# Kernel optimization log

Hardware: AMD Instinct MI355X
Metric: run time of the kernel (lower is better)

Reference implementation:

```python
import jax, jax.numpy as jnp
import numpy as np

B, LQ, LK, D = 8, 2048, 2048, 128
NEG = -100000.0


def setup_inputs() -> dict:
    key = jax.random.key(0)
    kq, kk, kv, km = jax.random.split(key, 4)
    q = jax.random.normal(kq, (B, LQ, D), dtype=jnp.float32)
    k = jax.random.normal(kk, (B, LK, D), dtype=jnp.float32)
    v = jax.random.normal(kv, (B, LK, D), dtype=jnp.float32)
    mask = jax.random.randint(km, (B, LQ, LK), 0, 2, dtype=jnp.int32)
    return {"q": q, "k": k, "v": v, "mask": mask}


def reference(q, k, v, mask):
    # atten_score = q @ k^T / sqrt(d)   [B, Lq, Lk]
    scores = jnp.einsum("bqd,bkd->bqk", q, k) / jnp.sqrt(jnp.float32(q.shape[-1]))
    # mask_mod == 2: additive mask, masked positions pushed to large negative
    scores = scores + mask.astype(jnp.float32) * NEG
    # sigmoid instead of softmax (no normalization across keys)
    attn = jax.nn.sigmoid(scores)
    return jnp.einsum("bqk,bkd->bqd", attn, v)
```

## Files before the change

### kernel.cpp

```cpp
#include <hip/hip_runtime.h>
#include <hip/hip_bf16.h>

#define B_   8
#define LQ_  2048
#define LK_  2048
#define D_   128
#define QBLK 64
#define KBLK 64
#define THREADS 512
#define SCALE 0.08838834764831845f
#define NEGL2E (-1.44269504088896340736f * SCALE)

typedef __attribute__((ext_vector_type(8))) __bf16 bf16x8;
typedef __attribute__((ext_vector_type(4))) float  f32x4;
typedef __attribute__((ext_vector_type(4))) float  fx4;
typedef __attribute__((ext_vector_type(4))) int    i32x4;

__global__ __launch_bounds__(256)
void kprep(const float* __restrict__ k, __bf16* __restrict__ kb)
{
    size_t i = ((size_t)blockIdx.x * 256 + threadIdx.x) * 8;
    fx4 a = *(const fx4*)(k + i);
    fx4 b = *(const fx4*)(k + i + 4);
    bf16x8 w;
#pragma unroll
    for (int j = 0; j < 4; ++j) { w[j] = (__bf16)a[j]; w[4 + j] = (__bf16)b[j]; }
    *(bf16x8*)(kb + i) = w;
}

__global__ __launch_bounds__(128)
void vprep(const float* __restrict__ v, __bf16* __restrict__ vt)
{
    const int b  = blockIdx.x & 7;
    const int k0 = (blockIdx.x >> 3) * 64;
    const int d  = threadIdx.x;
    const float* vb = v + ((size_t)b * LK_ + k0) * D_ + d;
    __bf16* vr = vt + ((size_t)b * D_ + d) * LK_ + k0;
#pragma unroll
    for (int grp = 0; grp < 2; ++grp) {
#pragma unroll
        for (int g = 0; g < 4; ++g) {
            bf16x8 w;
#pragma unroll
            for (int e = 0; e < 8; ++e) {
                int h = e >> 2, j = e & 3;
                int key = grp * 32 + h * 16 + g * 4 + j;
                w[e] = (__bf16)vb[(size_t)key * D_];
            }
            *(bf16x8*)(vr + grp * 32 + g * 8) = w;
        }
    }
}

__global__ __launch_bounds__(THREADS, 2)
void sigattn_main(const float* __restrict__ q, const int* __restrict__ mask,
                  const __bf16* __restrict__ Kb, const __bf16* __restrict__ Vt,
                  float* __restrict__ out)
{
    __shared__ float red[64 * 132];

    const int tid  = threadIdx.x;
    const int lane = tid & 63;
    const int l15  = lane & 15;
    const int g    = lane >> 4;
    const int wid  = tid >> 6;
    const int qg   = wid & 1;
    const int kg   = (wid >> 1) & 1;
    const int tp   = wid >> 2;

    const int bid   = blockIdx.x;
    const int b     = bid & 7;
    const int q0    = (bid >> 3) * QBLK;
    const int qbase = qg * 32;

    const float*  qb = q    + ((size_t)b * LQ_ + q0) * D_;
    const int*    mb = mask + ((size_t)b * LQ_ + q0) * LK_;
    const __bf16* kb = Kb   + (size_t)b * LK_ * D_;
    const __bf16* vt = Vt   + (size_t)b * D_ * LK_;
    float*        ob = out  + ((size_t)b * LQ_ + q0) * D_;

    bf16x8 qfrag[2][4];
#pragma unroll
    for (int qq = 0; qq < 2; ++qq) {
        const float* qrow = qb + (size_t)(qbase + qq * 16 + l15) * D_;
#pragma unroll
        for (int dblk = 0; dblk < 4; ++dblk) {
            fx4 f0 = *(const fx4*)(qrow + dblk * 32 + g * 8);
            fx4 f1 = *(const fx4*)(qrow + dblk * 32 + g * 8 + 4);
            bf16x8 w;
#pragma unroll
            for (int j = 0; j < 4; ++j) { w[j] = (__bf16)f0[j]; w[4 + j] = (__bf16)f1[j]; }
            qfrag[qq][dblk] = w;
        }
    }

    f32x4 oacc[2][8];
#pragma unroll
    for (int qq = 0; qq < 2; ++qq)
#pragma unroll
        for (int nb = 0; nb < 8; ++nb) oacc[qq][nb] = (f32x4){0.f, 0.f, 0.f, 0.f};

    const int* mr[2];
    mr[0] = mb + (size_t)(qbase + l15) * LK_ + kg * 32 + 4 * g;
    mr[1] = mr[0] + (size_t)16 * LK_;

    int kt = tp * KBLK;
    i32x4 mcur[2][2];
#pragma unroll
    for (int qq = 0; qq < 2; ++qq)
#pragma unroll
        for (int ksl = 0; ksl < 2; ++ksl)
            mcur[qq][ksl] = __builtin_nontemporal_load((const i32x4*)(mr[qq] + kt + ksl * 16));

    for (int i = 0; i < 16; ++i, kt += 2 * KBLK) {
        const int ktp = (i < 15) ? kt + 2 * KBLK : kt;

        i32x4 mnxt[2][2];
#pragma unroll
        for (int qq = 0; qq < 2; ++qq)
#pragma unroll
            for (int ksl = 0; ksl < 2; ++ksl)
                mnxt[qq][ksl] = __builtin_nontemporal_load((const i32x4*)(mr[qq] + ktp + ksl * 16));

        bf16x8 kfr[2][4];
#pragma unroll
        for (int ksl = 0; ksl < 2; ++ksl)
#pragma unroll
            for (int dblk = 0; dblk < 4; ++dblk)
                kfr[ksl][dblk] = *(const bf16x8*)(kb + (size_t)(kt + kg * 32 + ksl * 16 + l15) * D_ + dblk * 32 + g * 8);

        bf16x8 vfr[8];
#pragma unroll
        for (int nb = 0; nb < 8; ++nb)
            vfr[nb] = *(const bf16x8*)(vt + (size_t)(nb * 16 + l15) * LK_ + kt + kg * 32 + g * 8);

        f32x4 sacc[2][2];
#pragma unroll
        for (int qq = 0; qq < 2; ++qq)
#pragma unroll
            for (int ksl = 0; ksl < 2; ++ksl)
                sacc[qq][ksl] = (f32x4){0.f, 0.f, 0.f, 0.f};
#pragma unroll
        for (int ksl = 0; ksl < 2; ++ksl)
#pragma unroll
            for (int dblk = 0; dblk < 4; ++dblk) {
                bf16x8 a = kfr[ksl][dblk];
#pragma unroll
                for (int qq = 0; qq < 2; ++qq)
                    sacc[qq][ksl] = __builtin_amdgcn_mfma_f32_16x16x32_bf16(a, qfrag[qq][dblk], sacc[qq][ksl], 0, 0, 0);
            }

        bf16x8 pfrag[2];
#pragma unroll
        for (int qq = 0; qq < 2; ++qq)
#pragma unroll
            for (int ksl = 0; ksl < 2; ++ksl)
#pragma unroll
                for (int r = 0; r < 4; ++r) {
                    float e = exp2f(sacc[qq][ksl][r] * NEGL2E);
                    float p = __builtin_amdgcn_rcpf(1.0f + e);
                    p = (mcur[qq][ksl][r] != 0) ? 0.0f : p;
                    pfrag[qq][ksl * 4 + r] = (__bf16)p;
                }

#pragma unroll
        for (int nb = 0; nb < 8; ++nb)
#pragma unroll
            for (int qq = 0; qq < 2; ++qq)
                oacc[qq][nb] = __builtin_amdgcn_mfma_f32_16x16x32_bf16(pfrag[qq], vfr[nb], oacc[qq][nb], 0, 0, 0);

#pragma unroll
        for (int qq = 0; qq < 2; ++qq)
#pragma unroll
            for (int ksl = 0; ksl < 2; ++ksl) mcur[qq][ksl] = mnxt[qq][ksl];
    }

    if (tp == 0 && kg == 0) {
#pragma unroll
        for (int qq = 0; qq < 2; ++qq)
#pragma unroll
            for (int nb = 0; nb < 8; ++nb)
#pragma unroll
                for (int r = 0; r < 4; ++r)
                    red[(qbase + qq * 16 + 4 * g + r) * 132 + nb * 16 + l15] = oacc[qq][nb][r];
    }
    __syncthreads();
    if (tp == 0 && kg == 1) {
#pragma unroll
        for (int qq = 0; qq < 2; ++qq)
#pragma unroll
            for (int nb = 0; nb < 8; ++nb)
#pragma unroll
                for (int r = 0; r < 4; ++r)
                    red[(qbase + qq * 16 + 4 * g + r) * 132 + nb * 16 + l15] += oacc[qq][nb][r];
    }
    __syncthreads();
    if (tp == 1 && kg == 0) {
#pragma unroll
        for (int qq = 0; qq < 2; ++qq)
#pragma unroll
            for (int nb = 0; nb < 8; ++nb)
#pragma unroll
                for (int r = 0; r < 4; ++r)
                    red[(qbase + qq * 16 + 4 * g + r) * 132 + nb * 16 + l15] += oacc[qq][nb][r];
    }
    __syncthreads();
    if (tp == 1 && kg == 1) {
#pragma unroll
        for (int qq = 0; qq < 2; ++qq)
#pragma unroll
            for (int nb = 0; nb < 8; ++nb)
#pragma unroll
                for (int r = 0; r < 4; ++r)
                    red[(qbase + qq * 16 + 4 * g + r) * 132 + nb * 16 + l15] += oacc[qq][nb][r];
    }
    __syncthreads();
#pragma unroll
    for (int i2 = 0; i2 < 4; ++i2) {
        int idx = tid + i2 * THREADS;
        int row = idx >> 5, c4 = idx & 31;
        fx4 val = *(const fx4*)(red + row * 132 + c4 * 4);
        __builtin_nontemporal_store(val, (fx4*)(ob + (size_t)row * D_ + c4 * 4));
    }
}

extern "C" void kernel_launch(void* const* d_in, const int* in_sizes, int n_in,
                              void* d_out, int out_size, void* d_ws, size_t ws_size,
                              hipStream_t stream) {
    const float* q    = (const float*)d_in[0];
    const float* k    = (const float*)d_in[1];
    const float* v    = (const float*)d_in[2];
    const int*   mask = (const int*)d_in[3];
    float*       out  = (float*)d_out;

    __bf16* Kb = (__bf16*)d_ws;
    __bf16* Vt = (__bf16*)d_ws + (size_t)2097152;

    kprep<<<dim3(1024), dim3(256), 0, stream>>>(k, Kb);
    vprep<<<dim3(256), dim3(128), 0, stream>>>(v, Vt);
    sigattn_main<<<dim3(256), dim3(THREADS), 0, stream>>>(q, mask, Kb, Vt, out);
}
```

Before: 271.6 us.

## Pre-pack K/V into MFMA fragment order and stage mask bits through LDS

K and V are now pre-packed into per-lane MFMA fragment order, so each wave reads contiguous 1 KB chunks instead of strided rows. The mask is read with coalesced row-wise loads, compressed to 4-bit nibbles, and double-buffered in shared memory, with a barrier every iteration. K fragments for the next step are prefetched in registers. This should improve the coalescing of mask and K/V loads, at the cost of a per-iteration block barrier and extra LDS traffic.

```diff
diff --git a/kernel.cpp b/kernel.cpp
--- a/kernel.cpp
+++ b/kernel.cpp
@@ -6,10 +6,9 @@
 #define LK_  2048
 #define D_   128
 #define QBLK 64
-#define KBLK 64
 #define THREADS 512
-#define SCALE 0.08838834764831845f
-#define NEGL2E (-1.44269504088896340736f * SCALE)
+#define NITER 16
+#define NEGL2E (-0.12755004910797864f)
 
 typedef __attribute__((ext_vector_type(8))) __bf16 bf16x8;
 typedef __attribute__((ext_vector_type(4))) float  f32x4;
@@ -17,47 +16,46 @@
 typedef __attribute__((ext_vector_type(4))) int    i32x4;
 
 __global__ __launch_bounds__(256)
-void kprep(const float* __restrict__ k, __bf16* __restrict__ kb)
+void kprep(const float* __restrict__ k, __bf16* __restrict__ kp)
 {
-    size_t i = ((size_t)blockIdx.x * 256 + threadIdx.x) * 8;
-    fx4 a = *(const fx4*)(k + i);
-    fx4 b = *(const fx4*)(k + i + 4);
+    int id   = blockIdx.x * 256 + threadIdx.x;
+    int lane = id & 63;
+    int f    = id >> 6;
+    int dblk = f & 3, kk = (f >> 2) & 127, b = f >> 9;
+    const float* src = k + ((size_t)b * LK_ + kk * 16 + (lane & 15)) * D_
+                         + dblk * 32 + (lane >> 4) * 8;
+    fx4 f0 = *(const fx4*)src;
+    fx4 f1 = *(const fx4*)(src + 4);
     bf16x8 w;
 #pragma unroll
-    for (int j = 0; j < 4; ++j) { w[j] = (__bf16)a[j]; w[4 + j] = (__bf16)b[j]; }
-    *(bf16x8*)(kb + i) = w;
-}
-
-__global__ __launch_bounds__(128)
-void vprep(const float* __restrict__ v, __bf16* __restrict__ vt)
+    for (int j = 0; j < 4; ++j) { w[j] = (__bf16)f0[j]; w[4 + j] = (__bf16)f1[j]; }
+    *(bf16x8*)(kp + (size_t)f * 512 + lane * 8) = w;
+}
+
+__global__ __launch_bounds__(256)
+void vprep(const float* __restrict__ v, __bf16* __restrict__ vp)
 {
-    const int b  = blockIdx.x & 7;
-    const int k0 = (blockIdx.x >> 3) * 64;
-    const int d  = threadIdx.x;
-    const float* vb = v + ((size_t)b * LK_ + k0) * D_ + d;
-    __bf16* vr = vt + ((size_t)b * D_ + d) * LK_ + k0;
-#pragma unroll
-    for (int grp = 0; grp < 2; ++grp) {
-#pragma unroll
-        for (int g = 0; g < 4; ++g) {
-            bf16x8 w;
-#pragma unroll
-            for (int e = 0; e < 8; ++e) {
-                int h = e >> 2, j = e & 3;
-                int key = grp * 32 + h * 16 + g * 4 + j;
-                w[e] = (__bf16)vb[(size_t)key * D_];
-            }
-            *(bf16x8*)(vr + grp * 32 + g * 8) = w;
-        }
-    }
+    int id   = blockIdx.x * 256 + threadIdx.x;
+    int lane = id & 63;
+    int f    = id >> 6;
+    int nb = f & 7, ck = (f >> 3) & 63, b = f >> 9;
+    int l15 = lane & 15, g = lane >> 4;
+    bf16x8 w;
+#pragma unroll
+    for (int e = 0; e < 8; ++e) {
+        int key = ck * 32 + (e >> 2) * 16 + g * 4 + (e & 3);
+        w[e] = (__bf16)v[((size_t)b * LK_ + key) * D_ + nb * 16 + l15];
+    }
+    *(bf16x8*)(vp + (size_t)f * 512 + lane * 8) = w;
 }
 
 __global__ __launch_bounds__(THREADS, 2)
 void sigattn_main(const float* __restrict__ q, const int* __restrict__ mask,
-                  const __bf16* __restrict__ Kb, const __bf16* __restrict__ Vt,
+                  const __bf16* __restrict__ Kp, const __bf16* __restrict__ Vp,
                   float* __restrict__ out)
 {
-    __shared__ float red[64 * 132];
+    __shared__ __align__(16) char smem[64 * 132 * 4];
+    unsigned char* bitsbuf = (unsigned char*)smem;
 
     const int tid  = threadIdx.x;
     const int lane = tid & 63;
@@ -65,18 +63,17 @@
     const int g    = lane >> 4;
     const int wid  = tid >> 6;
     const int qg   = wid & 1;
-    const int kg   = (wid >> 1) & 1;
-    const int tp   = wid >> 2;
-
-    const int bid   = blockIdx.x;
-    const int b     = bid & 7;
-    const int q0    = (bid >> 3) * QBLK;
+    const int kq   = wid >> 1;
     const int qbase = qg * 32;
+
+    const int bid = blockIdx.x;
+    const int b   = bid & 7;
+    const int q0  = (bid >> 3) * QBLK;
 
     const float*  qb = q    + ((size_t)b * LQ_ + q0) * D_;
     const int*    mb = mask + ((size_t)b * LQ_ + q0) * LK_;
-    const __bf16* kb = Kb   + (size_t)b * LK_ * D_;
-    const __bf16* vt = Vt   + (size_t)b * D_ * LK_;
+    const __bf16* kp = Kp + (size_t)b * 262144;
+    const __bf16* vp = Vp + (size_t)b * 262144;
     float*        ob = out  + ((size_t)b * LQ_ + q0) * D_;
 
     bf16x8 qfrag[2][4];
@@ -94,74 +91,95 @@
         }
     }
 
+    const int prow = wid * 8 + (lane >> 5);
+    const int pk4  = lane & 31;
+    const int* mrow = mb + (size_t)prow * LK_ + pk4 * 4;
+
+    {
+        i32x4 m4[4];
+#pragma unroll
+        for (int j = 0; j < 4; ++j)
+            m4[j] = __builtin_nontemporal_load((const i32x4*)(mrow + (size_t)(j * 2) * LK_));
+#pragma unroll
+        for (int j = 0; j < 4; ++j) {
+            unsigned int nib = (m4[j][0] != 0 ? 1u : 0u) | (m4[j][1] != 0 ? 2u : 0u)
+                             | (m4[j][2] != 0 ? 4u : 0u) | (m4[j][3] != 0 ? 8u : 0u);
+            bitsbuf[(prow + j * 2) * 40 + pk4] = (unsigned char)nib;
+        }
+    }
+    bf16x8 Kc[2][4];
+#pragma unroll
+    for (int ksl = 0; ksl < 2; ++ksl)
+#pragma unroll
+        for (int dblk = 0; dblk < 4; ++dblk)
+            Kc[ksl][dblk] = *(const bf16x8*)(kp + (size_t)(((kq * 2 + ksl) * 4 + dblk)) * 512 + lane * 8);
+
+    asm volatile("s_waitcnt lgkmcnt(0)\n\ts_barrier" ::: "memory");
+
     f32x4 oacc[2][8];
 #pragma unroll
     for (int qq = 0; qq < 2; ++qq)
 #pragma unroll
         for (int nb = 0; nb < 8; ++nb) oacc[qq][nb] = (f32x4){0.f, 0.f, 0.f, 0.f};
 
-    const int* mr[2];
-    mr[0] = mb + (size_t)(qbase + l15) * LK_ + kg * 32 + 4 * g;
-    mr[1] = mr[0] + (size_t)16 * LK_;
-
-    int kt = tp * KBLK;
-    i32x4 mcur[2][2];
-#pragma unroll
-    for (int qq = 0; qq < 2; ++qq)
+    for (int i = 0; i < NITER; ++i) {
+        const bool more = (i + 1 < NITER);
+
+        bf16x8 vfr[8];
+#pragma unroll
+        for (int nb = 0; nb < 8; ++nb)
+            vfr[nb] = *(const bf16x8*)(vp + (size_t)(((i * 4 + kq) * 8 + nb)) * 512 + lane * 8);
+
+        i32x4 m4[4];
+        if (more) {
+#pragma unroll
+            for (int j = 0; j < 4; ++j)
+                m4[j] = __builtin_nontemporal_load(
+                    (const i32x4*)(mrow + (size_t)(i + 1) * 128 + (size_t)(j * 2) * LK_));
+        }
+
+        f32x4 sacc[2][2];
+#pragma unroll
+        for (int qq = 0; qq < 2; ++qq)
+#pragma unroll
+            for (int ksl = 0; ksl < 2; ++ksl) sacc[qq][ksl] = (f32x4){0.f, 0.f, 0.f, 0.f};
 #pragma unroll
         for (int ksl = 0; ksl < 2; ++ksl)
-            mcur[qq][ksl] = __builtin_nontemporal_load((const i32x4*)(mr[qq] + kt + ksl * 16));
-
-    for (int i = 0; i < 16; ++i, kt += 2 * KBLK) {
-        const int ktp = (i < 15) ? kt + 2 * KBLK : kt;
-
-        i32x4 mnxt[2][2];
-#pragma unroll
-        for (int qq = 0; qq < 2; ++qq)
-#pragma unroll
-            for (int ksl = 0; ksl < 2; ++ksl)
-                mnxt[qq][ksl] = __builtin_nontemporal_load((const i32x4*)(mr[qq] + ktp + ksl * 16));
-
-        bf16x8 kfr[2][4];
-#pragma unroll
-        for (int ksl = 0; ksl < 2; ++ksl)
-#pragma unroll
-            for (int dblk = 0; dblk < 4; ++dblk)
-                kfr[ksl][dblk] = *(const bf16x8*)(kb + (size_t)(kt + kg * 32 + ksl * 16 + l15) * D_ + dblk * 32 + g * 8);
-
-        bf16x8 vfr[8];
-#pragma unroll
-        for (int nb = 0; nb < 8; ++nb)
-            vfr[nb] = *(const bf16x8*)(vt + (size_t)(nb * 16 + l15) * LK_ + kt + kg * 32 + g * 8);
-
-        f32x4 sacc[2][2];
-#pragma unroll
-        for (int qq = 0; qq < 2; ++qq)
-#pragma unroll
-            for (int ksl = 0; ksl < 2; ++ksl)
-                sacc[qq][ksl] = (f32x4){0.f, 0.f, 0.f, 0.f};
-#pragma unroll
-        for (int ksl = 0; ksl < 2; ++ksl)
 #pragma unroll
             for (int dblk = 0; dblk < 4; ++dblk) {
-                bf16x8 a = kfr[ksl][dblk];
+                bf16x8 a = Kc[ksl][dblk];
 #pragma unroll
                 for (int qq = 0; qq < 2; ++qq)
                     sacc[qq][ksl] = __builtin_amdgcn_mfma_f32_16x16x32_bf16(a, qfrag[qq][dblk], sacc[qq][ksl], 0, 0, 0);
             }
 
+        bf16x8 Kn[2][4];
+        if (more) {
+#pragma unroll
+            for (int ksl = 0; ksl < 2; ++ksl)
+#pragma unroll
+                for (int dblk = 0; dblk < 4; ++dblk)
+                    Kn[ksl][dblk] = *(const bf16x8*)(kp + (size_t)((((i + 1) * 8 + kq * 2 + ksl) * 4 + dblk)) * 512 + lane * 8);
+        }
+
         bf16x8 pfrag[2];
 #pragma unroll
-        for (int qq = 0; qq < 2; ++qq)
-#pragma unroll
-            for (int ksl = 0; ksl < 2; ++ksl)
+        for (int qq = 0; qq < 2; ++qq) {
+            const int rrow = (qbase + qq * 16 + l15) * 40;
+            unsigned int b0 = bitsbuf[(i & 1) * 2560 + rrow + kq * 8 + g];
+            unsigned int b1 = bitsbuf[(i & 1) * 2560 + rrow + kq * 8 + 4 + g];
+#pragma unroll
+            for (int ksl = 0; ksl < 2; ++ksl) {
+                unsigned int bb = ksl ? b1 : b0;
 #pragma unroll
                 for (int r = 0; r < 4; ++r) {
                     float e = exp2f(sacc[qq][ksl][r] * NEGL2E);
                     float p = __builtin_amdgcn_rcpf(1.0f + e);
-                    p = (mcur[qq][ksl][r] != 0) ? 0.0f : p;
+                    p = ((bb >> r) & 1u) ? 0.0f : p;
                     pfrag[qq][ksl * 4 + r] = (__bf16)p;
                 }
+            }
+        }
 
 #pragma unroll
         for (int nb = 0; nb < 8; ++nb)
@@ -169,13 +187,29 @@
             for (int qq = 0; qq < 2; ++qq)
                 oacc[qq][nb] = __builtin_amdgcn_mfma_f32_16x16x32_bf16(pfrag[qq], vfr[nb], oacc[qq][nb], 0, 0, 0);
 
-#pragma unroll
-        for (int qq = 0; qq < 2; ++qq)
-#pragma unroll
-            for (int ksl = 0; ksl < 2; ++ksl) mcur[qq][ksl] = mnxt[qq][ksl];
-    }
-
-    if (tp == 0 && kg == 0) {
+        if (more) {
+#pragma unroll
+            for (int j = 0; j < 4; ++j) {
+                unsigned int nib = (m4[j][0] != 0 ? 1u : 0u) | (m4[j][1] != 0 ? 2u : 0u)
+                                 | (m4[j][2] != 0 ? 4u : 0u) | (m4[j][3] != 0 ? 8u : 0u);
+                bitsbuf[((i + 1) & 1) * 2560 + (prow + j * 2) * 40 + pk4] = (unsigned char)nib;
+            }
+        }
+
+        asm volatile("s_waitcnt lgkmcnt(0)\n\ts_barrier" ::: "memory");
+
+        if (more) {
+#pragma unroll
+            for (int ksl = 0; ksl < 2; ++ksl)
+#pragma unroll
+                for (int dblk = 0; dblk < 4; ++dblk)
+                    Kc[ksl][dblk] = Kn[ksl][dblk];
+        }
+    }
+
+    __syncthreads();
+    float* red = (float*)smem;
+    if (kq == 0) {
 #pragma unroll
         for (int qq = 0; qq < 2; ++qq)
 #pragma unroll
@@ -185,7 +219,7 @@
                     red[(qbase + qq * 16 + 4 * g + r) * 132 + nb * 16 + l15] = oacc[qq][nb][r];
     }
     __syncthreads();
-    if (tp == 0 && kg == 1) {
+    if (kq == 1) {
 #pragma unroll
         for (int qq = 0; qq < 2; ++qq)
 #pragma unroll
@@ -195,7 +229,7 @@
                     red[(qbase + qq * 16 + 4 * g + r) * 132 + nb * 16 + l15] += oacc[qq][nb][r];
     }
     __syncthreads();
-    if (tp == 1 && kg == 0) {
+    if (kq == 2) {
 #pragma unroll
         for (int qq = 0; qq < 2; ++qq)
 #pragma unroll
@@ -205,7 +239,7 @@
                     red[(qbase + qq * 16 + 4 * g + r) * 132 + nb * 16 + l15] += oacc[qq][nb][r];
     }
     __syncthreads();
-    if (tp == 1 && kg == 1) {
+    if (kq == 3) {
 #pragma unroll
         for (int qq = 0; qq < 2; ++qq)
 #pragma unroll
@@ -233,10 +267,10 @@
     const int*   mask = (const int*)d_in[3];
     float*       out  = (float*)d_out;
 
-    __bf16* Kb = (__bf16*)d_ws;
-    __bf16* Vt = (__bf16*)d_ws + (size_t)2097152;
-
-    kprep<<<dim3(1024), dim3(256), 0, stream>>>(k, Kb);
-    vprep<<<dim3(256), dim3(128), 0, stream>>>(v, Vt);
-    sigattn_main<<<dim3(256), dim3(THREADS), 0, stream>>>(q, mask, Kb, Vt, out);
-}
+    __bf16* Kp = (__bf16*)d_ws;
+    __bf16* Vp = (__bf16*)d_ws + (size_t)2097152;
+
+    kprep<<<dim3(1024), dim3(256), 0, stream>>>(k, Kp);
+    vprep<<<dim3(1024), dim3(256), 0, stream>>>(v, Vp);
+    sigattn_main<<<dim3(256), dim3(THREADS), 0, stream>>>(q, mask, Kp, Vp, out);
+}
```

After: 233.9 us. 13.9% less time.
